# Kernel tuning notes

Hardware: AMD Instinct MI355X
Metric: run time of the kernel (lower is better)

Reference implementation:

```python
import jax, jax.numpy as jnp
import numpy as np

N_NODES = 100000
N_EDGES = 800000
HIDDEN = 128
BN_EPS = 1e-5


def setup_inputs() -> dict:
    key = jax.random.key(0)
    k1, k2, k3 = jax.random.split(key, 3)
    x = jax.random.normal(k1, (N_NODES, HIDDEN), dtype=jnp.float32)
    edge_index = jax.random.randint(k2, (2, N_EDGES), 0, N_NODES, dtype=jnp.int64)
    # Glorot-style init for the GCN linear weight
    W = jax.random.normal(k3, (HIDDEN, HIDDEN), dtype=jnp.float32) / np.sqrt(HIDDEN)
    b = jnp.zeros((HIDDEN,), dtype=jnp.float32)
    gamma = jnp.ones((HIDDEN,), dtype=jnp.float32)
    beta = jnp.zeros((HIDDEN,), dtype=jnp.float32)
    return {"x": x, "edge_index": edge_index, "W": W, "b": b, "gamma": gamma, "beta": beta}


def reference(x, edge_index, W, b, gamma, beta):
    N = x.shape[0]
    xw = x @ W  # [N, d] linear transform first (PyG order)

    # add self-loops
    loops = jnp.arange(N, dtype=edge_index.dtype)
    row = jnp.concatenate([edge_index[0], loops])  # source
    col = jnp.concatenate([edge_index[1], loops])  # target

    # symmetric degree normalization on A~ = A + I
    deg = jax.ops.segment_sum(jnp.ones_like(col, dtype=x.dtype), col, num_segments=N)
    dinv = jax.lax.rsqrt(jnp.maximum(deg, 1.0))  # deg >= 1 due to self-loops
    norm = dinv[row] * dinv[col]  # [E+N]

    # gather -> scale -> scatter-add aggregation
    msgs = xw[row] * norm[:, None]  # [E+N, d]
    agg = jax.ops.segment_sum(msgs, col, num_segments=N) + b  # [N, d]

    # BatchNorm1d (batch statistics, biased variance) + ReLU; Dropout is identity (eval)
    mean = jnp.mean(agg, axis=0)
    var = jnp.var(agg, axis=0)
    h = (agg - mean) * jax.lax.rsqrt(var + BN_EPS) * gamma + beta
    return jax.nn.relu(h)
```

## Files before the change

kernel.cpp:

```cpp
#include <hip/hip_runtime.h>
#include <cstddef>

#define HIDDEN 128
#define BN_EPS 1e-5f
#define KS 136
#define BKT 64

typedef __attribute__((ext_vector_type(8))) short short8;
typedef __attribute__((ext_vector_type(4))) float float4v;
typedef __attribute__((ext_vector_type(4))) unsigned uint4v;

__device__ inline unsigned bf16_rne(float f) {
    unsigned u = __float_as_uint(f);
    return (u + 0x7fff + ((u >> 16) & 1)) >> 16;
}
__device__ inline unsigned pack2_bf16(float a, float b) {
    return bf16_rne(a) | (bf16_rne(b) << 16);
}

__global__ void k_count(const int* __restrict__ col, const int* __restrict__ row,
                        int* __restrict__ cnt, int* bucket, int E) {
    int e = blockIdx.x * 256 + threadIdx.x;
    if (e < E) {
        int c = col[e];
        int r = row[e];
        int p = atomicAdd(&cnt[c], 1);
        if (p < BKT) bucket[(size_t)c * BKT + p] = r;
    }
}

__global__ __launch_bounds__(256) void k_gemm(const float* __restrict__ x,
                                              const float* __restrict__ W,
                                              const int* __restrict__ cnt,
                                              unsigned short* __restrict__ xus, int N) {
    __shared__ unsigned short lA[128 * KS];
    __shared__ unsigned short lB[128 * KS];
    int tid = threadIdx.x;
    int row0 = blockIdx.x * 128;
    int wv = tid >> 6;
    int lane = tid & 63;
    int l15 = lane & 15;
    int lq = lane >> 4;

    for (int it = 0; it < 16; ++it) {
        int idx4 = it * 256 + tid;
        int m = idx4 >> 5, c4 = idx4 & 31;
        int grow = row0 + m;
        float4 v = make_float4(0.f, 0.f, 0.f, 0.f);
        if (grow < N) v = ((const float4*)x)[(size_t)grow * 32 + c4];
        uint2 pk;
        pk.x = pack2_bf16(v.x, v.y);
        pk.y = pack2_bf16(v.z, v.w);
        *(uint2*)&lA[m * KS + c4 * 4] = pk;
    }
    for (int it = 0; it < 16; ++it) {
        int idx4 = it * 256 + tid;
        int k = idx4 >> 5, n4 = idx4 & 31;
        float4 v = ((const float4*)W)[(size_t)k * 32 + n4];
        int n = n4 * 4;
        lB[(n + 0) * KS + k] = (unsigned short)bf16_rne(v.x);
        lB[(n + 1) * KS + k] = (unsigned short)bf16_rne(v.y);
        lB[(n + 2) * KS + k] = (unsigned short)bf16_rne(v.z);
        lB[(n + 3) * KS + k] = (unsigned short)bf16_rne(v.w);
    }
    __syncthreads();

    float4v acc[2][8];
#pragma unroll
    for (int i = 0; i < 2; ++i)
#pragma unroll
        for (int j = 0; j < 8; ++j) acc[i][j] = (float4v){0.f, 0.f, 0.f, 0.f};

#pragma unroll
    for (int kc = 0; kc < 4; ++kc) {
        int ko = kc * 32 + lq * 8;
        short8 a0 = *(const short8*)&lA[(wv * 32 + l15) * KS + ko];
        short8 a1 = *(const short8*)&lA[(wv * 32 + 16 + l15) * KS + ko];
        short8 bfr[8];
#pragma unroll
        for (int nt = 0; nt < 8; ++nt)
            bfr[nt] = *(const short8*)&lB[(nt * 16 + l15) * KS + ko];
#pragma unroll
        for (int nt = 0; nt < 8; ++nt) {
            acc[0][nt] = __builtin_amdgcn_mfma_f32_16x16x32_bf16(a0, bfr[nt], acc[0][nt], 0, 0, 0);
            acc[1][nt] = __builtin_amdgcn_mfma_f32_16x16x32_bf16(a1, bfr[nt], acc[1][nt], 0, 0, 0);
        }
    }

    __syncthreads();

#pragma unroll
    for (int mt = 0; mt < 2; ++mt) {
#pragma unroll
        for (int reg = 0; reg < 4; ++reg) {
            int rl = wv * 32 + mt * 16 + lq * 4 + reg;
            int r = row0 + rl;
            float d = 0.f;
            if (r < N) d = rsqrtf((float)(cnt[r] + 1));
#pragma unroll
            for (int nt = 0; nt < 8; ++nt)
                lA[rl * KS + nt * 16 + l15] = (unsigned short)bf16_rne(acc[mt][nt][reg] * d);
        }
    }
    __syncthreads();

    for (int it = 0; it < 8; ++it) {
        int idx = it * 256 + tid;
        int r = idx >> 4, c16 = idx & 15;
        int grow = row0 + r;
        if (grow < N) {
            uint4v v = *(const uint4v*)&lA[r * KS + c16 * 8];
            *((uint4v*)(xus + (size_t)grow * 128) + c16) = v;
        }
    }
}

__global__ __launch_bounds__(256) void k_gather(const unsigned* __restrict__ xu,
                                                const int* __restrict__ cnt,
                                                const float* __restrict__ b,
                                                unsigned* aggsrc,
                                                float* __restrict__ bn, int N) {
    int tid = threadIdx.x;
    int lane = tid & 63;
    int w = (blockIdx.x * 256 + tid) >> 6;
    int nw = (gridDim.x * 256) >> 6;
    float2 bb = ((const float2*)b)[lane];
    float2 s = make_float2(0.f, 0.f), qq = make_float2(0.f, 0.f);

    const int* bkt = (const int*)aggsrc;

    int i = w;
    int deg = 0;
    unsigned uself = 0;
    int pf[16];
#pragma unroll
    for (int k = 0; k < 16; ++k) pf[k] = 0;
    if (i < N) {
        deg = cnt[i];
        uself = xu[(size_t)i * 64 + lane];
        const int4* bp = (const int4*)(bkt + (size_t)i * BKT);
        int4 q0 = bp[0], q1 = bp[1], q2 = bp[2], q3 = bp[3];
        pf[0] = q0.x; pf[1] = q0.y; pf[2]  = q0.z; pf[3]  = q0.w;
        pf[4] = q1.x; pf[5] = q1.y; pf[6]  = q1.z; pf[7]  = q1.w;
        pf[8] = q2.x; pf[9] = q2.y; pf[10] = q2.z; pf[11] = q2.w;
        pf[12] = q3.x; pf[13] = q3.y; pf[14] = q3.z; pf[15] = q3.w;
    }

    while (i < N) {
        int inext = i + nw;
        int ndeg = 0;
        unsigned nself = 0;
        int npf[16];
#pragma unroll
        for (int k = 0; k < 16; ++k) npf[k] = 0;
        if (inext < N) {
            ndeg = cnt[inext];
            nself = xu[(size_t)inext * 64 + lane];
            const int4* bp = (const int4*)(bkt + (size_t)inext * BKT);
            int4 q0 = bp[0], q1 = bp[1], q2 = bp[2], q3 = bp[3];
            npf[0] = q0.x; npf[1] = q0.y; npf[2]  = q0.z; npf[3]  = q0.w;
            npf[4] = q1.x; npf[5] = q1.y; npf[6]  = q1.z; npf[7]  = q1.w;
            npf[8] = q2.x; npf[9] = q2.y; npf[10] = q2.z; npf[11] = q2.w;
            npf[12] = q3.x; npf[13] = q3.y; npf[14] = q3.z; npf[15] = q3.w;
        }

        int d = __builtin_amdgcn_readfirstlane(deg);
        if (d > BKT) d = BKT;
        float di = rsqrtf((float)(d + 1));
        float ax = __uint_as_float(uself << 16);
        float ay = __uint_as_float(uself & 0xffff0000u);

        if (d > 0) {
            unsigned u[8];
#pragma unroll
            for (int k = 0; k < 8; ++k) {
                int rk = (k < d) ? pf[k] : pf[0];
                u[k] = xu[(size_t)rk * 64 + lane];
            }
#pragma unroll
            for (int k = 0; k < 8; ++k) {
                unsigned uu = (k < d) ? u[k] : 0u;
                ax += __uint_as_float(uu << 16);
                ay += __uint_as_float(uu & 0xffff0000u);
            }
        }
        if (d > 8) {
            unsigned u[8];
#pragma unroll
            for (int k = 0; k < 8; ++k) {
                int rk = (8 + k < d) ? pf[8 + k] : pf[0];
                u[k] = xu[(size_t)rk * 64 + lane];
            }
#pragma unroll
            for (int k = 0; k < 8; ++k) {
                unsigned uu = (8 + k < d) ? u[k] : 0u;
                ax += __uint_as_float(uu << 16);
                ay += __uint_as_float(uu & 0xffff0000u);
            }
        }
        if (d > 16) {
            const int* bp = bkt + (size_t)i * BKT;
            int j = 16;
            for (; j + 8 <= d; j += 8) {
                int r0 = bp[j + 0], r1 = bp[j + 1], r2 = bp[j + 2], r3 = bp[j + 3];
                int r4 = bp[j + 4], r5 = bp[j + 5], r6 = bp[j + 6], r7 = bp[j + 7];
                unsigned u0 = xu[(size_t)r0 * 64 + lane];
                unsigned u1 = xu[(size_t)r1 * 64 + lane];
                unsigned u2 = xu[(size_t)r2 * 64 + lane];
                unsigned u3 = xu[(size_t)r3 * 64 + lane];
                unsigned u4 = xu[(size_t)r4 * 64 + lane];
                unsigned u5 = xu[(size_t)r5 * 64 + lane];
                unsigned u6 = xu[(size_t)r6 * 64 + lane];
                unsigned u7 = xu[(size_t)r7 * 64 + lane];
                ax += __uint_as_float(u0 << 16) + __uint_as_float(u1 << 16)
                    + __uint_as_float(u2 << 16) + __uint_as_float(u3 << 16);
                ay += __uint_as_float(u0 & 0xffff0000u) + __uint_as_float(u1 & 0xffff0000u)
                    + __uint_as_float(u2 & 0xffff0000u) + __uint_as_float(u3 & 0xffff0000u);
                ax += __uint_as_float(u4 << 16) + __uint_as_float(u5 << 16)
                    + __uint_as_float(u6 << 16) + __uint_as_float(u7 << 16);
                ay += __uint_as_float(u4 & 0xffff0000u) + __uint_as_float(u5 & 0xffff0000u)
                    + __uint_as_float(u6 & 0xffff0000u) + __uint_as_float(u7 & 0xffff0000u);
            }
            if (j < d) {
                int last = d - 1;
                int r[7];
#pragma unroll
                for (int k = 0; k < 7; ++k) {
                    int jk = j + k;
                    r[k] = bp[jk < d ? jk : last];
                }
                unsigned u[7];
#pragma unroll
                for (int k = 0; k < 7; ++k) u[k] = xu[(size_t)r[k] * 64 + lane];
#pragma unroll
                for (int k = 0; k < 7; ++k) {
                    unsigned uu = (j + k < d) ? u[k] : 0u;
                    ax += __uint_as_float(uu << 16);
                    ay += __uint_as_float(uu & 0xffff0000u);
                }
            }
        }

        float ox = fmaf(ax, di, bb.x);
        float oy = fmaf(ay, di, bb.y);
        aggsrc[(size_t)i * 64 + lane] = pack2_bf16(ox, oy);
        s.x += ox;
        s.y += oy;
        qq.x = fmaf(ox, ox, qq.x);
        qq.y = fmaf(oy, oy, qq.y);

        i = inext;
        deg = ndeg;
        uself = nself;
#pragma unroll
        for (int k = 0; k < 16; ++k) pf[k] = npf[k];
    }

    __shared__ float ssum[HIDDEN];
    __shared__ float ssq[HIDDEN];
    if (tid < HIDDEN) { ssum[tid] = 0.f; ssq[tid] = 0.f; }
    __syncthreads();
    atomicAdd(&ssum[2 * lane],     s.x);
    atomicAdd(&ssum[2 * lane + 1], s.y);
    atomicAdd(&ssq[2 * lane],      qq.x);
    atomicAdd(&ssq[2 * lane + 1],  qq.y);
    __syncthreads();
    if (tid < HIDDEN) {
        atomicAdd(&bn[tid],          ssum[tid]);
        atomicAdd(&bn[HIDDEN + tid], ssq[tid]);
    }
}

__global__ __launch_bounds__(256) void k_apply(const unsigned* __restrict__ agg,
                                               float* __restrict__ out,
                                               const float* __restrict__ bn,
                                               const float* __restrict__ gamma,
                                               const float* __restrict__ beta,
                                               int total8, float invN) {
    __shared__ float sc[HIDDEN], sh[HIDDEN];
    int tid = threadIdx.x;
    if (tid < HIDDEN) {
        float mean = bn[tid] * invN;
        float var = bn[HIDDEN + tid] * invN - mean * mean;
        float inv = rsqrtf(var + BN_EPS);
        float g = gamma[tid] * inv;
        sc[tid] = g;
        sh[tid] = beta[tid] - mean * g;
    }
    __syncthreads();
    int idx = blockIdx.x * 256 + tid;
    if (idx < total8) {
        uint2 u = ((const uint2*)agg)[idx];
        int c = (idx & 31) * 4;
        float4 v;
        v.x = __uint_as_float(u.x << 16);
        v.y = __uint_as_float(u.x & 0xffff0000u);
        v.z = __uint_as_float(u.y << 16);
        v.w = __uint_as_float(u.y & 0xffff0000u);
        v.x = fmaxf(fmaf(v.x, sc[c],     sh[c]),     0.f);
        v.y = fmaxf(fmaf(v.y, sc[c + 1], sh[c + 1]), 0.f);
        v.z = fmaxf(fmaf(v.z, sc[c + 2], sh[c + 2]), 0.f);
        v.w = fmaxf(fmaf(v.w, sc[c + 3], sh[c + 3]), 0.f);
        ((float4*)out)[idx] = v;
    }
}

extern "C" void kernel_launch(void* const* d_in, const int* in_sizes, int n_in,
                              void* d_out, int out_size, void* d_ws, size_t ws_size,
                              hipStream_t stream) {
    const float* x     = (const float*)d_in[0];
    const int*   edges = (const int*)d_in[1];
    const float* W     = (const float*)d_in[2];
    const float* b     = (const float*)d_in[3];
    const float* gamma = (const float*)d_in[4];
    const float* beta  = (const float*)d_in[5];
    float* out = (float*)d_out;

    int N = in_sizes[0] / HIDDEN;
    int E = in_sizes[1] / 2;
    const int* row = edges;
    const int* col = edges + E;

    char* p = (char*)d_ws;
    unsigned* xu  = (unsigned*)p; p += (size_t)N * 64 * sizeof(unsigned);
    unsigned* agg = (unsigned*)p; p += (size_t)N * 64 * sizeof(unsigned);
    int*   cnt    = (int*)p;   p += (size_t)N * sizeof(int);
    float* bn     = (float*)p; p += 256 * sizeof(float);

    size_t zbytes = (size_t)N * sizeof(int) + 256 * sizeof(float);

    dim3 blk(256);
    hipMemsetAsync(cnt, 0, zbytes, stream);
    k_count<<<dim3((E + 255) / 256), blk, 0, stream>>>(col, row, cnt, (int*)agg, E);
    k_gemm<<<dim3((N + 127) / 128), blk, 0, stream>>>(x, W, cnt, (unsigned short*)xu, N);
    k_gather<<<dim3(2048), blk, 0, stream>>>(xu, cnt, b, agg, bn, N);
    int total8 = N * 32;
    k_apply<<<dim3((total8 + 255) / 256), blk, 0, stream>>>(agg, out, bn, gamma, beta,
                                                            total8, 1.0f / (float)N);
}
```

Baseline: 279.3 us.

## Fuse gather and BatchNorm apply into one cooperative kernel with grid sync

Merges the gather/aggregation kernel and the BatchNorm+ReLU apply kernel into a single cooperative launch that uses a grid-wide barrier between the statistics accumulation and the normalization pass. This removes one kernel launch and its launch gap. Each wave then re-reads its own aggregated rows, so they may still be in cache. If the cooperative launch fails, the code falls back to the original two kernels. The grid barrier adds synchronization cost, and the launch_bounds occupancy hint may limit registers available to the gather body.

```diff
diff --git a/kernel.cpp b/kernel.cpp
--- a/kernel.cpp
+++ b/kernel.cpp
@@ -1,5 +1,8 @@
 #include <hip/hip_runtime.h>
+#include <hip/hip_cooperative_groups.h>
 #include <cstddef>
+
+namespace cg = cooperative_groups;
 
 #define HIDDEN 128
 #define BN_EPS 1e-5f
@@ -115,15 +118,11 @@
     }
 }
 
-__global__ __launch_bounds__(256) void k_gather(const unsigned* __restrict__ xu,
-                                                const int* __restrict__ cnt,
-                                                const float* __restrict__ b,
-                                                unsigned* aggsrc,
-                                                float* __restrict__ bn, int N) {
-    int tid = threadIdx.x;
-    int lane = tid & 63;
-    int w = (blockIdx.x * 256 + tid) >> 6;
-    int nw = (gridDim.x * 256) >> 6;
+__device__ inline void gather_body(const unsigned* __restrict__ xu,
+                                   const int* __restrict__ cnt,
+                                   const float* __restrict__ b,
+                                   unsigned* aggsrc, float* bn,
+                                   int N, int tid, int lane, int w, int nw) {
     float2 bb = ((const float2*)b)[lane];
     float2 s = make_float2(0.f, 0.f), qq = make_float2(0.f, 0.f);
 
@@ -271,6 +270,59 @@
     }
 }
 
+__global__ __launch_bounds__(256, 8) void k_gather_apply(
+        const unsigned* __restrict__ xu, const int* __restrict__ cnt,
+        const float* __restrict__ b, unsigned* aggsrc, float* bn,
+        float* __restrict__ out, const float* __restrict__ gamma,
+        const float* __restrict__ beta, int N, float invN) {
+    cg::grid_group g = cg::this_grid();
+    int tid = threadIdx.x;
+    int lane = tid & 63;
+    int w = (blockIdx.x * 256 + tid) >> 6;
+    int nw = (gridDim.x * 256) >> 6;
+
+    gather_body(xu, cnt, b, aggsrc, bn, N, tid, lane, w, nw);
+
+    g.sync();
+
+    __shared__ float sc[HIDDEN], sh[HIDDEN];
+    if (tid < HIDDEN) {
+        float sum = atomicAdd(&bn[tid], 0.0f);
+        float sq  = atomicAdd(&bn[HIDDEN + tid], 0.0f);
+        float mean = sum * invN;
+        float var = sq * invN - mean * mean;
+        float inv = rsqrtf(var + BN_EPS);
+        float gmm = gamma[tid] * inv;
+        sc[tid] = gmm;
+        sh[tid] = beta[tid] - mean * gmm;
+    }
+    __syncthreads();
+
+    float scx = sc[2 * lane], shx = sh[2 * lane];
+    float scy = sc[2 * lane + 1], shy = sh[2 * lane + 1];
+    for (int i = w; i < N; i += nw) {
+        unsigned u = aggsrc[(size_t)i * 64 + lane];
+        float vx = __uint_as_float(u << 16);
+        float vy = __uint_as_float(u & 0xffff0000u);
+        float2 o;
+        o.x = fmaxf(fmaf(vx, scx, shx), 0.f);
+        o.y = fmaxf(fmaf(vy, scy, shy), 0.f);
+        ((float2*)out)[(size_t)i * 64 + lane] = o;
+    }
+}
+
+__global__ __launch_bounds__(256) void k_gather(const unsigned* __restrict__ xu,
+                                                const int* __restrict__ cnt,
+                                                const float* __restrict__ b,
+                                                unsigned* aggsrc,
+                                                float* bn, int N) {
+    int tid = threadIdx.x;
+    int lane = tid & 63;
+    int w = (blockIdx.x * 256 + tid) >> 6;
+    int nw = (gridDim.x * 256) >> 6;
+    gather_body(xu, cnt, b, aggsrc, bn, N, tid, lane, w, nw);
+}
+
 __global__ __launch_bounds__(256) void k_apply(const unsigned* __restrict__ agg,
                                                float* __restrict__ out,
                                                const float* __restrict__ bn,
@@ -329,12 +381,26 @@
 
     size_t zbytes = (size_t)N * sizeof(int) + 256 * sizeof(float);
 
+    int total8 = N * 32;
+    float invN = 1.0f / (float)N;
+    int* bucket = (int*)agg;
+    unsigned short* xus = (unsigned short*)xu;
+
     dim3 blk(256);
     hipMemsetAsync(cnt, 0, zbytes, stream);
-    k_count<<<dim3((E + 255) / 256), blk, 0, stream>>>(col, row, cnt, (int*)agg, E);
-    k_gemm<<<dim3((N + 127) / 128), blk, 0, stream>>>(x, W, cnt, (unsigned short*)xu, N);
-    k_gather<<<dim3(2048), blk, 0, stream>>>(xu, cnt, b, agg, bn, N);
-    int total8 = N * 32;
-    k_apply<<<dim3((total8 + 255) / 256), blk, 0, stream>>>(agg, out, bn, gamma, beta,
-                                                            total8, 1.0f / (float)N);
-}
+    k_count<<<dim3((E + 255) / 256), blk, 0, stream>>>(col, row, cnt, bucket, E);
+    k_gemm<<<dim3((N + 127) / 128), blk, 0, stream>>>(x, W, cnt, xus, N);
+
+    {
+        void* args[] = { (void*)&xu, (void*)&cnt, (void*)&b, (void*)&agg, (void*)&bn,
+                         (void*)&out, (void*)&gamma, (void*)&beta,
+                         (void*)&N, (void*)&invN };
+        hipError_t e = hipLaunchCooperativeKernel((const void*)k_gather_apply,
+                                                  dim3(2048), blk, args, 0, stream);
+        if (e != hipSuccess) {
+            k_gather<<<dim3(2048), blk, 0, stream>>>(xu, cnt, b, agg, bn, N);
+            k_apply<<<dim3((total8 + 255) / 256), blk, 0, stream>>>(agg, out, bn, gamma,
+                                                                    beta, total8, invN);
+        }
+    }
+}
```

Result: slower. 546.3 us (+95.6%).
